# Optimization experiments

Hardware: AMD Instinct MI355X
Metric: run time of the kernel (lower is better)

## Reference

```python
import jax, jax.numpy as jnp
import numpy as np

D_MODEL = 1024
NUM_HEADS = 16
D_K = D_MODEL // NUM_HEADS


def setup_inputs() -> dict:
    key = jax.random.key(0)
    ks = jax.random.split(key, 11)
    B, S = 2, 2048
    s = 1.0 / np.sqrt(D_MODEL)
    inp = {
        'q': jax.random.normal(ks[0], (B, S, D_MODEL), jnp.float32),
        'k': jax.random.normal(ks[1], (B, S, D_MODEL), jnp.float32),
        'v': jax.random.normal(ks[2], (B, S, D_MODEL), jnp.float32),
        'w_q': jax.random.normal(ks[3], (D_MODEL, D_MODEL), jnp.float32) * s,
        'b_q': jnp.zeros((D_MODEL,), jnp.float32),
        'w_k': jax.random.normal(ks[4], (D_MODEL, D_MODEL), jnp.float32) * s,
        'b_k': jnp.zeros((D_MODEL,), jnp.float32),
        'w_v': jax.random.normal(ks[5], (D_MODEL, D_MODEL), jnp.float32) * s,
        'b_v': jnp.zeros((D_MODEL,), jnp.float32),
        'w_o': jax.random.normal(ks[6], (D_MODEL, D_MODEL), jnp.float32) * s,
        'b_o': jnp.zeros((D_MODEL,), jnp.float32),
    }
    return inp


def reference(q, k, v, w_q, b_q, w_k, b_k, w_v, b_v, w_o, b_o):
    B, S, _ = q.shape
    # linear projections (torch Linear: x @ W.T + b)
    def proj(x, w, b):
        y = x @ w.T + b
        # [B, S, D] -> [B, H, S, d_k]
        return y.reshape(B, -1, NUM_HEADS, D_K).transpose(0, 2, 1, 3)

    Q = proj(q, w_q, b_q)
    K = proj(k, w_k, b_k)
    V = proj(v, w_v, b_v)

    scale = 1.0 / np.sqrt(D_K).astype(np.float32)
    scores = jnp.einsum('bhqd,bhkd->bhqk', Q, K) * scale  # [B,H,S,S]
    weights = jax.nn.softmax(scores, axis=-1)
    # dropout is identity in eval mode
    x = jnp.einsum('bhqk,bhkd->bhqd', weights, V)
    x = x.transpose(0, 2, 1, 3).reshape(B, S, NUM_HEADS * D_K)
    return x @ w_o.T + b_o
```

## Files before the change

### kernel.cpp

```cpp
#include <hip/hip_runtime.h>

typedef __attribute__((ext_vector_type(8))) short short8;
typedef __attribute__((ext_vector_type(4))) float f32x4;

#define NHEADS 16
#define DK 64
#define SEQ 2048
#define DMODEL 1024

__device__ __forceinline__ unsigned short f2bf(float f) {
  union { float f; unsigned int u; } c; c.f = f;
  unsigned int u = c.u;
  return (unsigned short)((u + 0x7FFFu + ((u >> 16) & 1u)) >> 16);
}

__device__ __forceinline__ float exp2_hw(float x) {
  float y;
  asm("v_exp_f32 %0, %1" : "=v"(y) : "v"(x));
  return y;
}

__device__ __forceinline__ unsigned int cvtpk_bf16(float lo, float hi) {
  unsigned int r;
  asm("v_cvt_pk_bf16_f32 %0, %1, %2" : "=v"(r) : "v"(lo), "v"(hi));
  return r;
}

__device__ __forceinline__ short8 ldg16(const unsigned short* p) {
  return *reinterpret_cast<const short8*>(p);
}

__device__ __forceinline__ void gload_lds16(const unsigned short* g, unsigned short* l) {
  __builtin_amdgcn_global_load_lds(
      (const __attribute__((address_space(1))) unsigned int*)g,
      (__attribute__((address_space(3))) unsigned int*)l, 16, 0, 0);
}

__global__ void cast_qkv(const float* __restrict__ a0, const float* __restrict__ a1,
                         const float* __restrict__ a2, unsigned short* __restrict__ d0,
                         unsigned short* __restrict__ d1, unsigned short* __restrict__ d2) {
  const float* s = blockIdx.y == 0 ? a0 : (blockIdx.y == 1 ? a1 : a2);
  unsigned short* d = blockIdx.y == 0 ? d0 : (blockIdx.y == 1 ? d1 : d2);
  int i = blockIdx.x * blockDim.x + threadIdx.x;
  float4 v = reinterpret_cast<const float4*>(s)[i];
  ushort4 o;
  o.x = f2bf(v.x); o.y = f2bf(v.y); o.z = f2bf(v.z); o.w = f2bf(v.w);
  reinterpret_cast<ushort4*>(d)[i] = o;
}

__global__ void cast_w4(const float* __restrict__ a0, const float* __restrict__ a1,
                        const float* __restrict__ a2, const float* __restrict__ a3,
                        unsigned short* __restrict__ d0, unsigned short* __restrict__ d1,
                        unsigned short* __restrict__ d2, unsigned short* __restrict__ d3) {
  const float* s = blockIdx.y == 0 ? a0 : (blockIdx.y == 1 ? a1 : (blockIdx.y == 2 ? a2 : a3));
  unsigned short* d = blockIdx.y == 0 ? d0 : (blockIdx.y == 1 ? d1 : (blockIdx.y == 2 ? d2 : d3));
  int i = blockIdx.x * blockDim.x + threadIdx.x;
  float4 v = reinterpret_cast<const float4*>(s)[i];
  ushort4 o;
  o.x = f2bf(v.x); o.y = f2bf(v.y); o.z = f2bf(v.z); o.w = f2bf(v.w);
  reinterpret_cast<ushort4*>(d)[i] = o;
}

__device__ __forceinline__ void gemm_core(const unsigned short* __restrict__ A,
                                          const unsigned short* __restrict__ W,
                                          unsigned short* As, unsigned short* Bs,
                                          int m0, int n0, f32x4 acc[4][2]) {
  const int t = threadIdx.x;
  const int lane = t & 63, w = t >> 6;
  const int wr = w >> 2, wc = w & 3;
  const int srow = t >> 2, scol = (t & 3) * 8;
  const int lr = lane >> 4, lc = lane & 15;
  for (int k0 = 0; k0 < DMODEL; k0 += 32) {
    __syncthreads();
    gload_lds16(A + (size_t)(m0 + srow) * DMODEL + k0 + scol, As + w * 512);
    gload_lds16(W + (size_t)(n0 + srow) * DMODEL + k0 + scol, Bs + w * 512);
    __syncthreads();
    short8 a[4], b[2];
#pragma unroll
    for (int i = 0; i < 4; ++i)
      a[i] = *reinterpret_cast<const short8*>(As + (wr * 64 + i * 16 + lc) * 32 + lr * 8);
#pragma unroll
    for (int i = 0; i < 2; ++i)
      b[i] = *reinterpret_cast<const short8*>(Bs + (wc * 32 + i * 16 + lc) * 32 + lr * 8);
#pragma unroll
    for (int mi = 0; mi < 4; ++mi)
#pragma unroll
      for (int ni = 0; ni < 2; ++ni)
        acc[mi][ni] = __builtin_amdgcn_mfma_f32_16x16x32_bf16(a[mi], b[ni], acc[mi][ni], 0, 0, 0);
  }
}

struct ProjPtrs {
  const unsigned short* A0; const unsigned short* A1; const unsigned short* A2;
  const unsigned short* W0; const unsigned short* W1; const unsigned short* W2;
  const float* bias0; const float* bias1; const float* bias2;
  unsigned short* dst0; unsigned short* dst1; unsigned short* dst2;
};

__global__ __launch_bounds__(512) void gemm_proj(ProjPtrs p) {
  __shared__ __align__(16) unsigned short As[4096];
  __shared__ __align__(16) unsigned short Bs[4096];
  const int mode = blockIdx.z;
  const unsigned short* A = mode == 0 ? p.A0 : (mode == 1 ? p.A1 : p.A2);
  const unsigned short* W = mode == 0 ? p.W0 : (mode == 1 ? p.W1 : p.W2);
  const float* bias = mode == 0 ? p.bias0 : (mode == 1 ? p.bias1 : p.bias2);
  unsigned short* dst = mode == 0 ? p.dst0 : (mode == 1 ? p.dst1 : p.dst2);
  const int m0 = blockIdx.y * 128, n0 = blockIdx.x * 128;
  f32x4 acc[4][2] = {};
  gemm_core(A, W, As, Bs, m0, n0, acc);
  const int lane = threadIdx.x & 63, w = threadIdx.x >> 6;
  const int wr = w >> 2, wc = w & 3;
  const int lr = lane >> 4, lc = lane & 15;
#pragma unroll
  for (int mi = 0; mi < 4; ++mi) {
#pragma unroll
    for (int ni = 0; ni < 2; ++ni) {
      const int cg = n0 + wc * 32 + ni * 16 + lc;
      const int rb = m0 + wr * 64 + mi * 16 + lr * 4;
      const float bv = bias[cg];
      const int h = cg >> 6, d = cg & 63;
      if (mode == 2) {
        const int bb = rb >> 11, s = rb & 2047;
        ushort4 pk;
        pk.x = f2bf(acc[mi][ni][0] + bv);
        pk.y = f2bf(acc[mi][ni][1] + bv);
        pk.z = f2bf(acc[mi][ni][2] + bv);
        pk.w = f2bf(acc[mi][ni][3] + bv);
        *reinterpret_cast<ushort4*>(dst + (((size_t)((bb * NHEADS + h) * DK + d)) << 11) + s) = pk;
      } else {
        const float sc = (mode == 0) ? 0.18033688f : 1.0f;
#pragma unroll
        for (int j = 0; j < 4; ++j) {
          const int rg = rb + j;
          const int bb = rg >> 11, s = rg & 2047;
          dst[((size_t)(bb * NHEADS + h) * SEQ + s) * DK + d] = f2bf((acc[mi][ni][j] + bv) * sc);
        }
      }
    }
  }
}

__global__ __launch_bounds__(512) void gemm_out(const unsigned short* __restrict__ A,
                                                const unsigned short* __restrict__ W,
                                                const float* __restrict__ bias,
                                                float* __restrict__ out) {
  __shared__ __align__(16) unsigned short As[4096];
  __shared__ __align__(16) unsigned short Bs[4096];
  const int m0 = blockIdx.y * 128, n0 = blockIdx.x * 128;
  f32x4 acc[4][2] = {};
  gemm_core(A, W, As, Bs, m0, n0, acc);
  const int lane = threadIdx.x & 63, w = threadIdx.x >> 6;
  const int wr = w >> 2, wc = w & 3;
  const int lr = lane >> 4, lc = lane & 15;
#pragma unroll
  for (int mi = 0; mi < 4; ++mi)
#pragma unroll
    for (int ni = 0; ni < 2; ++ni) {
      const int cg = n0 + wc * 32 + ni * 16 + lc;
      const int rb = m0 + wr * 64 + mi * 16 + lr * 4;
      const float bv = bias[cg];
#pragma unroll
      for (int j = 0; j < 4; ++j)
        out[(size_t)(rb + j) * DMODEL + cg] = acc[mi][ni][j] + bv;
    }
}

__global__ __launch_bounds__(256) void attn_fwd(const unsigned short* __restrict__ Qh,
                                                const unsigned short* __restrict__ Kh,
                                                const unsigned short* __restrict__ Vt,
                                                unsigned short* __restrict__ Oh) {
  __shared__ __align__(16) unsigned short Ktile[2][4096];
  __shared__ __align__(16) unsigned short Vtile[2][4096];
  __shared__ __align__(16) unsigned short P[4][32][76];
  const int t = threadIdx.x, w = t >> 6, lane = t & 63;
  const int bx = ((blockIdx.x & 7) << 6) | (blockIdx.x >> 3);
  const int bh = bx >> 4, qblk = bx & 15;
  const int q0 = qblk * 128 + w * 32;
  const unsigned short* Qp = Qh + (size_t)bh * SEQ * DK;
  const unsigned short* Kp = Kh + (size_t)bh * SEQ * DK;
  const unsigned short* Vp = Vt + (size_t)bh * DK * SEQ;
  const int r = lane & 15, g = lane >> 4;

  const short8 qa0 = ldg16(Qp + (size_t)(q0 + r) * DK + g * 8);
  const short8 qa1 = ldg16(Qp + (size_t)(q0 + r) * DK + 32 + g * 8);
  const short8 qb0 = ldg16(Qp + (size_t)(q0 + 16 + r) * DK + g * 8);
  const short8 qb1 = ldg16(Qp + (size_t)(q0 + 16 + r) * DK + 32 + g * 8);

  const int c0 = w * 64 + lane, c1 = c0 + 256;
  const int r0 = c0 >> 3, s0 = (c0 & 7) ^ (r0 & 7);
  const int r1 = c1 >> 3, s1 = (c1 & 7) ^ (r1 & 7);
  const unsigned short* ks0 = Kp + r0 * DK + s0 * 8;
  const unsigned short* ks1 = Kp + r1 * DK + s1 * 8;
  const unsigned short* vs0 = Vp + (size_t)r0 * SEQ + s0 * 8;
  const unsigned short* vs1 = Vp + (size_t)r1 * SEQ + s1 * 8;

  float mA = -1e30f, lA = 0.f, mB = -1e30f, lB = 0.f;
  f32x4 oA[4] = {}, oB[4] = {};

  const int sw0 = ((g ^ (r & 7)) << 3);
  const int sw1 = (((g + 4) ^ (r & 7)) << 3);
  char* prowA = (char*)&P[w][r][0];
  char* prowB = (char*)&P[w][16 + r][0];

  gload_lds16(ks0, &Ktile[0][w * 512]);
  gload_lds16(ks1, &Ktile[0][2048 + w * 512]);
  gload_lds16(vs0, &Vtile[0][w * 512]);
  gload_lds16(vs1, &Vtile[0][2048 + w * 512]);
  __syncthreads();

  int buf = 0;
  for (int kt = 0; kt < 32; ++kt) {
    if (kt < 31) {
      const int kvn = (kt + 1) * 64;
      gload_lds16(ks0 + kvn * DK, &Ktile[buf ^ 1][w * 512]);
      gload_lds16(ks1 + kvn * DK, &Ktile[buf ^ 1][2048 + w * 512]);
      gload_lds16(vs0 + kvn, &Vtile[buf ^ 1][w * 512]);
      gload_lds16(vs1 + kvn, &Vtile[buf ^ 1][2048 + w * 512]);
    }
    f32x4 sA[4] = {}, sB[4] = {};
#pragma unroll
    for (int nt = 0; nt < 4; ++nt) {
      const short8 k0 = *reinterpret_cast<const short8*>(&Ktile[buf][(nt * 16 + r) * 64 + sw0]);
      const short8 k1 = *reinterpret_cast<const short8*>(&Ktile[buf][(nt * 16 + r) * 64 + sw1]);
      sA[nt] = __builtin_amdgcn_mfma_f32_16x16x32_bf16(k0, qa0, sA[nt], 0, 0, 0);
      sA[nt] = __builtin_amdgcn_mfma_f32_16x16x32_bf16(k1, qa1, sA[nt], 0, 0, 0);
      sB[nt] = __builtin_amdgcn_mfma_f32_16x16x32_bf16(k0, qb0, sB[nt], 0, 0, 0);
      sB[nt] = __builtin_amdgcn_mfma_f32_16x16x32_bf16(k1, qb1, sB[nt], 0, 0, 0);
    }
    {
      f32x4 pm;
#pragma unroll
      for (int j = 0; j < 4; ++j)
        pm[j] = fmaxf(fmaxf(sA[0][j], sA[1][j]), fmaxf(sA[2][j], sA[3][j]));
      float pmax = fmaxf(fmaxf(pm[0], pm[1]), fmaxf(pm[2], pm[3]));
      pmax = fmaxf(pmax, __shfl_xor(pmax, 16));
      pmax = fmaxf(pmax, __shfl_xor(pmax, 32));
      if (!__all(pmax - mA <= 8.f)) {
        const float mn = fmaxf(mA, pmax);
        const float al = exp2_hw(mA - mn);
        mA = mn; lA *= al;
        float alj[4];
#pragma unroll
        for (int j = 0; j < 4; ++j) alj[j] = __shfl(al, 4 * g + j, 16);
#pragma unroll
        for (int nt = 0; nt < 4; ++nt)
#pragma unroll
          for (int j = 0; j < 4; ++j) oA[nt][j] *= alj[j];
      }
#pragma unroll
      for (int nt = 0; nt < 4; ++nt)
#pragma unroll
        for (int j = 0; j < 4; ++j) sA[nt][j] = exp2_hw(sA[nt][j] - mA);
      f32x4 s4;
#pragma unroll
      for (int j = 0; j < 4; ++j) s4[j] = (sA[0][j] + sA[1][j]) + (sA[2][j] + sA[3][j]);
      float sum = (s4[0] + s4[1]) + (s4[2] + s4[3]);
      sum += __shfl_xor(sum, 16);
      sum += __shfl_xor(sum, 32);
      lA += sum;
#pragma unroll
      for (int nt = 0; nt < 4; ++nt) {
        uint2 pk;
        pk.x = cvtpk_bf16(sA[nt][0], sA[nt][1]);
        pk.y = cvtpk_bf16(sA[nt][2], sA[nt][3]);
        *reinterpret_cast<uint2*>(prowA + nt * 32 + g * 8) = pk;
      }
    }
    {
      f32x4 pm;
#pragma unroll
      for (int j = 0; j < 4; ++j)
        pm[j] = fmaxf(fmaxf(sB[0][j], sB[1][j]), fmaxf(sB[2][j], sB[3][j]));
      float pmax = fmaxf(fmaxf(pm[0], pm[1]), fmaxf(pm[2], pm[3]));
      pmax = fmaxf(pmax, __shfl_xor(pmax, 16));
      pmax = fmaxf(pmax, __shfl_xor(pmax, 32));
      if (!__all(pmax - mB <= 8.f)) {
        const float mn = fmaxf(mB, pmax);
        const float al = exp2_hw(mB - mn);
        mB = mn; lB *= al;
        float alj[4];
#pragma unroll
        for (int j = 0; j < 4; ++j) alj[j] = __shfl(al, 4 * g + j, 16);
#pragma unroll
        for (int nt = 0; nt < 4; ++nt)
#pragma unroll
          for (int j = 0; j < 4; ++j) oB[nt][j] *= alj[j];
      }
#pragma unroll
      for (int nt = 0; nt < 4; ++nt)
#pragma unroll
        for (int j = 0; j < 4; ++j) sB[nt][j] = exp2_hw(sB[nt][j] - mB);
      f32x4 s4;
#pragma unroll
      for (int j = 0; j < 4; ++j) s4[j] = (sB[0][j] + sB[1][j]) + (sB[2][j] + sB[3][j]);
      float sum = (s4[0] + s4[1]) + (s4[2] + s4[3]);
      sum += __shfl_xor(sum, 16);
      sum += __shfl_xor(sum, 32);
      lB += sum;
#pragma unroll
      for (int nt = 0; nt < 4; ++nt) {
        uint2 pk;
        pk.x = cvtpk_bf16(sB[nt][0], sB[nt][1]);
        pk.y = cvtpk_bf16(sB[nt][2], sB[nt][3]);
        *reinterpret_cast<uint2*>(prowB + nt * 32 + g * 8) = pk;
      }
    }
    union { short8 v; unsigned long long q[2]; } pA0, pA1, pB0, pB1;
    pA0.q[0] = *reinterpret_cast<const unsigned long long*>(prowA + g * 16);
    pA0.q[1] = *reinterpret_cast<const unsigned long long*>(prowA + g * 16 + 8);
    pA1.q[0] = *reinterpret_cast<const unsigned long long*>(prowA + 64 + g * 16);
    pA1.q[1] = *reinterpret_cast<const unsigned long long*>(prowA + 64 + g * 16 + 8);
    pB0.q[0] = *reinterpret_cast<const unsigned long long*>(prowB + g * 16);
    pB0.q[1] = *reinterpret_cast<const unsigned long long*>(prowB + g * 16 + 8);
    pB1.q[0] = *reinterpret_cast<const unsigned long long*>(prowB + 64 + g * 16);
    pB1.q[1] = *reinterpret_cast<const unsigned long long*>(prowB + 64 + g * 16 + 8);
#pragma unroll
    for (int nt = 0; nt < 4; ++nt) {
      const short8 v0 = *reinterpret_cast<const short8*>(&Vtile[buf][(nt * 16 + r) * 64 + sw0]);
      const short8 v1 = *reinterpret_cast<const short8*>(&Vtile[buf][(nt * 16 + r) * 64 + sw1]);
      oA[nt] = __builtin_amdgcn_mfma_f32_16x16x32_bf16(pA0.v, v0, oA[nt], 0, 0, 0);
      oA[nt] = __builtin_amdgcn_mfma_f32_16x16x32_bf16(pA1.v, v1, oA[nt], 0, 0, 0);
      oB[nt] = __builtin_amdgcn_mfma_f32_16x16x32_bf16(pB0.v, v0, oB[nt], 0, 0, 0);
      oB[nt] = __builtin_amdgcn_mfma_f32_16x16x32_bf16(pB1.v, v1, oB[nt], 0, 0, 0);
    }
    __syncthreads();
    buf ^= 1;
  }

  const float invA = 1.f / lA, invB = 1.f / lB;
  float ivA[4], ivB[4];
#pragma unroll
  for (int j = 0; j < 4; ++j) {
    ivA[j] = __shfl(invA, 4 * g + j, 16);
    ivB[j] = __shfl(invB, 4 * g + j, 16);
  }
  const size_t ob = ((size_t)((bh >> 4) * SEQ + q0)) * DMODEL + (size_t)(bh & 15) * DK;
#pragma unroll
  for (int nt = 0; nt < 4; ++nt)
#pragma unroll
    for (int j = 0; j < 4; ++j) {
      Oh[ob + (size_t)(g * 4 + j) * DMODEL + nt * 16 + r] = f2bf(oA[nt][j] * ivA[j]);
      Oh[ob + (size_t)(16 + g * 4 + j) * DMODEL + nt * 16 + r] = f2bf(oB[nt][j] * ivB[j]);
    }
}

extern "C" void kernel_launch(void* const* d_in, const int* in_sizes, int n_in,
                              void* d_out, int out_size, void* d_ws, size_t ws_size,
                              hipStream_t stream) {
  const float* q   = (const float*)d_in[0];
  const float* k   = (const float*)d_in[1];
  const float* v   = (const float*)d_in[2];
  const float* w_q = (const float*)d_in[3];
  const float* b_q = (const float*)d_in[4];
  const float* w_k = (const float*)d_in[5];
  const float* b_k = (const float*)d_in[6];
  const float* w_v = (const float*)d_in[7];
  const float* b_v = (const float*)d_in[8];
  const float* w_o = (const float*)d_in[9];
  const float* b_o = (const float*)d_in[10];
  float* out = (float*)d_out;
  char* ws = (char*)d_ws;
  const size_t MB = (size_t)1 << 20;
  unsigned short* qc  = (unsigned short*)(ws + 0 * MB);
  unsigned short* kc  = (unsigned short*)(ws + 8 * MB);
  unsigned short* vc  = (unsigned short*)(ws + 16 * MB);
  unsigned short* wqc = (unsigned short*)(ws + 24 * MB);
  unsigned short* wkc = (unsigned short*)(ws + 26 * MB);
  unsigned short* wvc = (unsigned short*)(ws + 28 * MB);
  unsigned short* woc = (unsigned short*)(ws + 30 * MB);
  unsigned short* Qh  = (unsigned short*)(ws + 32 * MB);
  unsigned short* Kh  = (unsigned short*)(ws + 40 * MB);
  unsigned short* Vt  = (unsigned short*)(ws + 48 * MB);
  unsigned short* Oh  = (unsigned short*)(ws + 56 * MB);

  cast_qkv<<<dim3(4096, 3), 256, 0, stream>>>(q, k, v, qc, kc, vc);
  cast_w4<<<dim3(1024, 4), 256, 0, stream>>>(w_q, w_k, w_v, w_o, wqc, wkc, wvc, woc);

  ProjPtrs p;
  p.A0 = qc; p.A1 = kc; p.A2 = vc;
  p.W0 = wqc; p.W1 = wkc; p.W2 = wvc;
  p.bias0 = b_q; p.bias1 = b_k; p.bias2 = b_v;
  p.dst0 = Qh; p.dst1 = Kh; p.dst2 = Vt;
  gemm_proj<<<dim3(8, 32, 3), 512, 0, stream>>>(p);

  attn_fwd<<<512, 256, 0, stream>>>(Qh, Kh, Vt, Oh);

  gemm_out<<<dim3(8, 32), 512, 0, stream>>>(Oh, woc, b_o, out);
}
```

Before: 247.6 us.

## Double-buffer projection and output GEMMs and raise MFMA priority in attention

The projection and output GEMMs now double-buffer their LDS tiles, prefetching the next K-slice while the current one is computed, which leaves one barrier per iteration instead of two. Projection blocks drop to 256 threads with a 4x4 MFMA tile per wave, and the output GEMM moves to 128x64 tiles to double its block count. The attention kernel wraps its MFMA sections in s_setprio to favour matrix issue. The cost is double the LDS per block and more accumulator registers, which can lower occupancy.

Result: no change. 252.4 us (+1.9%).

```diff
diff --git a/kernel.cpp b/kernel.cpp
--- a/kernel.cpp
+++ b/kernel.cpp
@@ -61,35 +61,6 @@
   reinterpret_cast<ushort4*>(d)[i] = o;
 }
 
-__device__ __forceinline__ void gemm_core(const unsigned short* __restrict__ A,
-                                          const unsigned short* __restrict__ W,
-                                          unsigned short* As, unsigned short* Bs,
-                                          int m0, int n0, f32x4 acc[4][2]) {
-  const int t = threadIdx.x;
-  const int lane = t & 63, w = t >> 6;
-  const int wr = w >> 2, wc = w & 3;
-  const int srow = t >> 2, scol = (t & 3) * 8;
-  const int lr = lane >> 4, lc = lane & 15;
-  for (int k0 = 0; k0 < DMODEL; k0 += 32) {
-    __syncthreads();
-    gload_lds16(A + (size_t)(m0 + srow) * DMODEL + k0 + scol, As + w * 512);
-    gload_lds16(W + (size_t)(n0 + srow) * DMODEL + k0 + scol, Bs + w * 512);
-    __syncthreads();
-    short8 a[4], b[2];
-#pragma unroll
-    for (int i = 0; i < 4; ++i)
-      a[i] = *reinterpret_cast<const short8*>(As + (wr * 64 + i * 16 + lc) * 32 + lr * 8);
-#pragma unroll
-    for (int i = 0; i < 2; ++i)
-      b[i] = *reinterpret_cast<const short8*>(Bs + (wc * 32 + i * 16 + lc) * 32 + lr * 8);
-#pragma unroll
-    for (int mi = 0; mi < 4; ++mi)
-#pragma unroll
-      for (int ni = 0; ni < 2; ++ni)
-        acc[mi][ni] = __builtin_amdgcn_mfma_f32_16x16x32_bf16(a[mi], b[ni], acc[mi][ni], 0, 0, 0);
-  }
-}
-
 struct ProjPtrs {
   const unsigned short* A0; const unsigned short* A1; const unsigned short* A2;
   const unsigned short* W0; const unsigned short* W1; const unsigned short* W2;
@@ -97,25 +68,57 @@
   unsigned short* dst0; unsigned short* dst1; unsigned short* dst2;
 };
 
-__global__ __launch_bounds__(512) void gemm_proj(ProjPtrs p) {
-  __shared__ __align__(16) unsigned short As[4096];
-  __shared__ __align__(16) unsigned short Bs[4096];
+__global__ __launch_bounds__(256) void gemm_proj(ProjPtrs p) {
+  __shared__ __align__(16) unsigned short As[2][4096];
+  __shared__ __align__(16) unsigned short Bs[2][4096];
   const int mode = blockIdx.z;
   const unsigned short* A = mode == 0 ? p.A0 : (mode == 1 ? p.A1 : p.A2);
   const unsigned short* W = mode == 0 ? p.W0 : (mode == 1 ? p.W1 : p.W2);
   const float* bias = mode == 0 ? p.bias0 : (mode == 1 ? p.bias1 : p.bias2);
   unsigned short* dst = mode == 0 ? p.dst0 : (mode == 1 ? p.dst1 : p.dst2);
   const int m0 = blockIdx.y * 128, n0 = blockIdx.x * 128;
-  f32x4 acc[4][2] = {};
-  gemm_core(A, W, As, Bs, m0, n0, acc);
-  const int lane = threadIdx.x & 63, w = threadIdx.x >> 6;
-  const int wr = w >> 2, wc = w & 3;
+  const int t = threadIdx.x, lane = t & 63, w = t >> 6;
+  const int wr = w >> 1, wc = w & 1;
   const int lr = lane >> 4, lc = lane & 15;
+  const unsigned short* a_src0 = A + (size_t)(m0 + (t >> 2)) * DMODEL + (t & 3) * 8;
+  const unsigned short* a_src1 = A + (size_t)(m0 + 64 + (t >> 2)) * DMODEL + (t & 3) * 8;
+  const unsigned short* w_src0 = W + (size_t)(n0 + (t >> 2)) * DMODEL + (t & 3) * 8;
+  const unsigned short* w_src1 = W + (size_t)(n0 + 64 + (t >> 2)) * DMODEL + (t & 3) * 8;
+
+  f32x4 acc[4][4] = {};
+  gload_lds16(a_src0, &As[0][t * 8]);
+  gload_lds16(a_src1, &As[0][2048 + t * 8]);
+  gload_lds16(w_src0, &Bs[0][t * 8]);
+  gload_lds16(w_src1, &Bs[0][2048 + t * 8]);
+  __syncthreads();
+  int buf = 0;
+  for (int k0 = 0; k0 < DMODEL; k0 += 32) {
+    if (k0 < DMODEL - 32) {
+      const int kn = k0 + 32;
+      gload_lds16(a_src0 + kn, &As[buf ^ 1][t * 8]);
+      gload_lds16(a_src1 + kn, &As[buf ^ 1][2048 + t * 8]);
+      gload_lds16(w_src0 + kn, &Bs[buf ^ 1][t * 8]);
+      gload_lds16(w_src1 + kn, &Bs[buf ^ 1][2048 + t * 8]);
+    }
+    short8 a[4], b[4];
+#pragma unroll
+    for (int i = 0; i < 4; ++i) {
+      a[i] = *reinterpret_cast<const short8*>(&As[buf][(wr * 64 + i * 16 + lc) * 32 + lr * 8]);
+      b[i] = *reinterpret_cast<const short8*>(&Bs[buf][(wc * 64 + i * 16 + lc) * 32 + lr * 8]);
+    }
+#pragma unroll
+    for (int mi = 0; mi < 4; ++mi)
+#pragma unroll
+      for (int ni = 0; ni < 4; ++ni)
+        acc[mi][ni] = __builtin_amdgcn_mfma_f32_16x16x32_bf16(a[mi], b[ni], acc[mi][ni], 0, 0, 0);
+    __syncthreads();
+    buf ^= 1;
+  }
 #pragma unroll
   for (int mi = 0; mi < 4; ++mi) {
 #pragma unroll
-    for (int ni = 0; ni < 2; ++ni) {
-      const int cg = n0 + wc * 32 + ni * 16 + lc;
+    for (int ni = 0; ni < 4; ++ni) {
+      const int cg = n0 + wc * 64 + ni * 16 + lc;
       const int rb = m0 + wr * 64 + mi * 16 + lr * 4;
       const float bv = bias[cg];
       const int h = cg >> 6, d = cg & 63;
@@ -140,18 +143,48 @@
   }
 }
 
-__global__ __launch_bounds__(512) void gemm_out(const unsigned short* __restrict__ A,
+__global__ __launch_bounds__(256) void gemm_out(const unsigned short* __restrict__ A,
                                                 const unsigned short* __restrict__ W,
                                                 const float* __restrict__ bias,
                                                 float* __restrict__ out) {
-  __shared__ __align__(16) unsigned short As[4096];
-  __shared__ __align__(16) unsigned short Bs[4096];
-  const int m0 = blockIdx.y * 128, n0 = blockIdx.x * 128;
+  __shared__ __align__(16) unsigned short As[2][4096];
+  __shared__ __align__(16) unsigned short Bs[2][2048];
+  const int m0 = blockIdx.y * 128, n0 = blockIdx.x * 64;
+  const int t = threadIdx.x, lane = t & 63, w = t >> 6;
+  const int wr = w >> 1, wc = w & 1;
+  const int lr = lane >> 4, lc = lane & 15;
+  const unsigned short* a_src0 = A + (size_t)(m0 + (t >> 2)) * DMODEL + (t & 3) * 8;
+  const unsigned short* a_src1 = A + (size_t)(m0 + 64 + (t >> 2)) * DMODEL + (t & 3) * 8;
+  const unsigned short* w_src0 = W + (size_t)(n0 + (t >> 2)) * DMODEL + (t & 3) * 8;
+
   f32x4 acc[4][2] = {};
-  gemm_core(A, W, As, Bs, m0, n0, acc);
-  const int lane = threadIdx.x & 63, w = threadIdx.x >> 6;
-  const int wr = w >> 2, wc = w & 3;
-  const int lr = lane >> 4, lc = lane & 15;
+  gload_lds16(a_src0, &As[0][t * 8]);
+  gload_lds16(a_src1, &As[0][2048 + t * 8]);
+  gload_lds16(w_src0, &Bs[0][t * 8]);
+  __syncthreads();
+  int buf = 0;
+  for (int k0 = 0; k0 < DMODEL; k0 += 32) {
+    if (k0 < DMODEL - 32) {
+      const int kn = k0 + 32;
+      gload_lds16(a_src0 + kn, &As[buf ^ 1][t * 8]);
+      gload_lds16(a_src1 + kn, &As[buf ^ 1][2048 + t * 8]);
+      gload_lds16(w_src0 + kn, &Bs[buf ^ 1][t * 8]);
+    }
+    short8 a[4], b[2];
+#pragma unroll
+    for (int i = 0; i < 4; ++i)
+      a[i] = *reinterpret_cast<const short8*>(&As[buf][(wr * 64 + i * 16 + lc) * 32 + lr * 8]);
+#pragma unroll
+    for (int i = 0; i < 2; ++i)
+      b[i] = *reinterpret_cast<const short8*>(&Bs[buf][(wc * 32 + i * 16 + lc) * 32 + lr * 8]);
+#pragma unroll
+    for (int mi = 0; mi < 4; ++mi)
+#pragma unroll
+      for (int ni = 0; ni < 2; ++ni)
+        acc[mi][ni] = __builtin_amdgcn_mfma_f32_16x16x32_bf16(a[mi], b[ni], acc[mi][ni], 0, 0, 0);
+    __syncthreads();
+    buf ^= 1;
+  }
 #pragma unroll
   for (int mi = 0; mi < 4; ++mi)
 #pragma unroll
@@ -218,6 +251,7 @@
       gload_lds16(vs1 + kvn, &Vtile[buf ^ 1][2048 + w * 512]);
     }
     f32x4 sA[4] = {}, sB[4] = {};
+    __builtin_amdgcn_s_setprio(1);
 #pragma unroll
     for (int nt = 0; nt < 4; ++nt) {
       const short8 k0 = *reinterpret_cast<const short8*>(&Ktile[buf][(nt * 16 + r) * 64 + sw0]);
@@ -227,6 +261,7 @@
       sB[nt] = __builtin_amdgcn_mfma_f32_16x16x32_bf16(k0, qb0, sB[nt], 0, 0, 0);
       sB[nt] = __builtin_amdgcn_mfma_f32_16x16x32_bf16(k1, qb1, sB[nt], 0, 0, 0);
     }
+    __builtin_amdgcn_s_setprio(0);
     {
       f32x4 pm;
 #pragma unroll
@@ -314,6 +349,7 @@
     pB0.q[1] = *reinterpret_cast<const unsigned long long*>(prowB + g * 16 + 8);
     pB1.q[0] = *reinterpret_cast<const unsigned long long*>(prowB + 64 + g * 16);
     pB1.q[1] = *reinterpret_cast<const unsigned long long*>(prowB + 64 + g * 16 + 8);
+    __builtin_amdgcn_s_setprio(1);
 #pragma unroll
     for (int nt = 0; nt < 4; ++nt) {
       const short8 v0 = *reinterpret_cast<const short8*>(&Vtile[buf][(nt * 16 + r) * 64 + sw0]);
@@ -323,6 +359,7 @@
       oB[nt] = __builtin_amdgcn_mfma_f32_16x16x32_bf16(pB0.v, v0, oB[nt], 0, 0, 0);
       oB[nt] = __builtin_amdgcn_mfma_f32_16x16x32_bf16(pB1.v, v1, oB[nt], 0, 0, 0);
     }
+    __builtin_amdgcn_s_setprio(0);
     __syncthreads();
     buf ^= 1;
   }
@@ -381,9 +418,9 @@
   p.W0 = wqc; p.W1 = wkc; p.W2 = wvc;
   p.bias0 = b_q; p.bias1 = b_k; p.bias2 = b_v;
   p.dst0 = Qh; p.dst1 = Kh; p.dst2 = Vt;
-  gemm_proj<<<dim3(8, 32, 3), 512, 0, stream>>>(p);
+  gemm_proj<<<dim3(8, 32, 3), 256, 0, stream>>>(p);
 
   attn_fwd<<<512, 256, 0, stream>>>(Qh, Kh, Vt, Oh);
 
-  gemm_out<<<dim3(8, 32), 512, 0, stream>>>(Oh, woc, b_o, out);
-}
+  gemm_out<<<dim3(16, 32), 256, 0, stream>>>(Oh, woc, b_o, out);
+}
```
